# Optimization experiments

Hardware: AMD Instinct MI355X
Metric: run time of the kernel (lower is better)

Reference implementation:

```python
import jax, jax.numpy as jnp
import numpy as np

N = 50000      # nodes
E = 800000     # edges (avg degree 16)
D_IN = 128     # in_feats
D_OUT = 128    # out_feats
EPS = 1e-5     # LayerNorm eps


def setup_inputs() -> dict:
    key = jax.random.key(0)
    ks = jax.random.split(key, 8)
    stdv = 1.0 / np.sqrt(5 * D_IN)
    return {
        "h": jax.random.normal(ks[0], (N, D_IN), dtype=jnp.float32),
        "dist": jax.random.uniform(ks[1], (E,), dtype=jnp.float32),
        "W": jax.random.uniform(ks[2], (D_OUT, 5 * D_IN), minval=-stdv, maxval=stdv, dtype=jnp.float32),
        "b": jax.random.uniform(ks[3], (D_OUT,), minval=-stdv, maxval=stdv, dtype=jnp.float32),
        "gamma": jnp.ones((D_OUT,), dtype=jnp.float32),
        "beta": jnp.zeros((D_OUT,), dtype=jnp.float32),
        "src": jax.random.randint(ks[4], (E,), 0, N, dtype=jnp.int32),
        "dst": jax.random.randint(ks[5], (E,), 0, N, dtype=jnp.int32),
        "positions": jax.random.randint(ks[6], (E,), 0, 4, dtype=jnp.int32),
    }


def reference(h, dist, W, b, gamma, beta, src, dst, positions):
    n = h.shape[0]
    h_src = h[src]  # [E, D] gather once, reused by all four directions

    def direction(p):
        # edge-masked u_mul_e + sum aggregation to dst
        w = jnp.where(positions == p, dist, 0.0)
        return jax.ops.segment_sum(h_src * w[:, None], dst, num_segments=n)

    r = direction(0)   # right
    bt = direction(1)  # bottom
    l = direction(2)   # left
    t = direction(0)   # top (original code reuses positions == 0 — faithful)

    cat = jnp.concatenate([h, r, bt, l, t], axis=1)  # [N, 5D]
    z = cat @ W.T + b                                 # [N, D_OUT]
    mu = jnp.mean(z, axis=-1, keepdims=True)
    var = jnp.mean(jnp.square(z - mu), axis=-1, keepdims=True)
    z = (z - mu) * jax.lax.rsqrt(var + EPS) * gamma + beta
    return jax.nn.relu(z)
```

## Files before the change

### kernel.cpp

```cpp
#include <hip/hip_runtime.h>
#include <math.h>
#include <stdint.h>

constexpr int NN = 50000;
constexpr int EE = 800000;
constexpr int D  = 128;
constexpr int KK = 512;
constexpr int KA = 384;
constexpr int BM = 64;
constexpr int BK = 64;
constexpr int NPAD = 50048;
constexpr int CAP = 64;

typedef __attribute__((ext_vector_type(8)))  short bf16x8;
typedef __attribute__((ext_vector_type(16))) float f32x16;

__device__ inline unsigned short f2bf(float x) {
    unsigned u = __builtin_bit_cast(unsigned, x);
    unsigned r = (u + 0x7FFF + ((u >> 16) & 1)) >> 16;
    return (unsigned short)r;
}
__device__ inline float bf2f(unsigned short b) {
    unsigned u = ((unsigned)b) << 16;
    return __builtin_bit_cast(float, u);
}

__global__ __launch_bounds__(256) void prep_wfrag(const float* __restrict__ W,
                                                  unsigned short* __restrict__ Wfh,
                                                  unsigned short* __restrict__ Wfl)
{
    int tid = blockIdx.x * 256 + threadIdx.x;
    int ln  = tid & 31;
    int ksl = (tid >> 5) & 63;
    int cb  = tid >> 11;
    int col = cb * 32 + ln;
    short h8[8], l8[8];
#pragma unroll
    for (int j = 0; j < 8; ++j) {
        int k = ksl * 8 + j;
        float v = W[col * 640 + k];
        if (k >= 128 && k < 256) v += W[col * 640 + k + 384];
        unsigned short hb = f2bf(v);
        h8[j] = (short)hb;
        l8[j] = (short)f2bf(v - bf2f(hb));
    }
    *(bf16x8*)(Wfh + (size_t)tid * 8) = *(bf16x8*)h8;
    *(bf16x8*)(Wfl + (size_t)tid * 8) = *(bf16x8*)l8;
}

__global__ __launch_bounds__(256) void fill_bucket(const int* __restrict__ src,
                                                   const int* __restrict__ dst,
                                                   const int* __restrict__ pos,
                                                   const float* __restrict__ dist,
                                                   int* __restrict__ deg,
                                                   int2* __restrict__ bucket)
{
    int e = blockIdx.x * 256 + threadIdx.x;
    if (e >= EE) return;
    int p = pos[e];
    if (p == 3) return;
    int d_ = dst[e];
    int slot = atomicAdd(&deg[d_], 1);
    if (slot < CAP)
        bucket[(size_t)d_ * CAP + slot] =
            make_int2(src[e] | (p << 16), __float_as_int(dist[e]));
}

__global__ __launch_bounds__(256) void gather_agg(const float* __restrict__ h,
                                                  const int2* __restrict__ bucket,
                                                  const int* __restrict__ deg,
                                                  unsigned short* __restrict__ Xhi)
{
    int node = (blockIdx.x * 256 + threadIdx.x) >> 6;
    if (node >= NN) return;
    int lane = threadIdx.x & 63;
    int n = deg[node];
    if (n > CAP) n = CAP;

    int2 mreg = (lane < n) ? bucket[(size_t)node * CAP + lane] : make_int2(0, 0);

    float2 a0 = {0.f, 0.f}, a1 = {0.f, 0.f}, a2 = {0.f, 0.f};
    int e = 0;
    for (; e + 8 <= n; e += 8) {
        float2 v[8];
        float  wq[8];
        int    pq[8];
#pragma unroll
        for (int j = 0; j < 8; ++j) {
            int mx = __shfl(mreg.x, e + j);
            int my = __shfl(mreg.y, e + j);
            pq[j] = mx >> 16;
            wq[j] = __int_as_float(my);
            v[j]  = ((const float2*)(h + (size_t)(mx & 0xFFFF) * D))[lane];
        }
#pragma unroll
        for (int j = 0; j < 8; ++j) {
            float w0 = (pq[j] == 0) ? wq[j] : 0.f;
            float w1 = (pq[j] == 1) ? wq[j] : 0.f;
            float w2 = (pq[j] == 2) ? wq[j] : 0.f;
            a0.x = fmaf(v[j].x, w0, a0.x); a0.y = fmaf(v[j].y, w0, a0.y);
            a1.x = fmaf(v[j].x, w1, a1.x); a1.y = fmaf(v[j].y, w1, a1.y);
            a2.x = fmaf(v[j].x, w2, a2.x); a2.y = fmaf(v[j].y, w2, a2.y);
        }
    }
    for (; e < n; ++e) {
        int mx = __shfl(mreg.x, e);
        int my = __shfl(mreg.y, e);
        float w = __int_as_float(my);
        float2 v = ((const float2*)(h + (size_t)(mx & 0xFFFF) * D))[lane];
        float w0 = ((mx >> 16) == 0) ? w : 0.f;
        float w1 = ((mx >> 16) == 1) ? w : 0.f;
        float w2 = ((mx >> 16) == 2) ? w : 0.f;
        a0.x = fmaf(v.x, w0, a0.x); a0.y = fmaf(v.y, w0, a0.y);
        a1.x = fmaf(v.x, w1, a1.x); a1.y = fmaf(v.y, w1, a1.y);
        a2.x = fmaf(v.x, w2, a2.x); a2.y = fmaf(v.y, w2, a2.y);
    }

    size_t base = (size_t)node * KA + lane * 2;
    float2 as[3] = {a0, a1, a2};
#pragma unroll
    for (int p = 0; p < 3; ++p) {
        unsigned short h0 = f2bf(as[p].x), h1 = f2bf(as[p].y);
        *(unsigned*)(Xhi + base + p * 128) = (unsigned)h0 | ((unsigned)h1 << 16);
    }
}

__global__ __launch_bounds__(256, 3) void gemm_mfma(
    const float* __restrict__ h,
    const unsigned short* __restrict__ Xhi,
    const unsigned short* __restrict__ Wfh, const unsigned short* __restrict__ Wfl,
    const float* __restrict__ bias, const float* __restrict__ gamma,
    const float* __restrict__ beta, float* __restrict__ out)
{
    __shared__ __align__(16) short lds[2 * BM * BK];

    const int t = threadIdx.x;
    const int l = t & 63;
    const int w = t >> 6;
    const int wr = (w & 1) * 32;
    const int wch = (w >> 1);
    const int row0 = blockIdx.x * BM;
    const int ln = l & 31;
    const int hs = l >> 5;

    int crow[2], cks[2], clof[2];
#pragma unroll
    for (int p = 0; p < 2; ++p) {
        int idx = t + 256 * p;
        crow[p] = idx >> 3;
        cks[p]  = idx & 7;
        clof[p] = crow[p] * 64 + ((cks[p] ^ (crow[p] & 7)) * 8);
    }

    float4 pa[4];

    auto LOADA = [&](int kt) {
        const int k0 = kt * BK;
        if (kt < 2) {
#pragma unroll
            for (int p = 0; p < 2; ++p) {
                int grow = row0 + crow[p];
                if (grow < NN) {
                    const float* hp = h + (size_t)grow * D + k0 + cks[p] * 8;
                    pa[2 * p]     = *(const float4*)hp;
                    pa[2 * p + 1] = *(const float4*)(hp + 4);
                } else {
                    pa[2 * p]     = make_float4(0, 0, 0, 0);
                    pa[2 * p + 1] = make_float4(0, 0, 0, 0);
                }
            }
        } else {
#pragma unroll
            for (int p = 0; p < 2; ++p) {
                size_t ga = (size_t)(row0 + crow[p]) * KA + (k0 - 128) + cks[p] * 8;
                pa[p] = *(const float4*)(Xhi + ga);
            }
        }
    };

    auto STOREA = [&](int kt, short* buf) {
        if (kt < 2) {
#pragma unroll
            for (int p = 0; p < 2; ++p) {
                const float* f0 = (const float*)&pa[2 * p];
                const float* f1 = (const float*)&pa[2 * p + 1];
                short b8[8];
#pragma unroll
                for (int j = 0; j < 4; ++j) {
                    b8[j]     = (short)f2bf(f0[j]);
                    b8[4 + j] = (short)f2bf(f1[j]);
                }
                *(bf16x8*)(buf + clof[p]) = *(bf16x8*)b8;
            }
        } else {
#pragma unroll
            for (int p = 0; p < 2; ++p)
                *(float4*)(buf + clof[p]) = pa[p];
        }
    };

    f32x16 acc[2];
#pragma unroll
    for (int cb = 0; cb < 2; ++cb)
#pragma unroll
        for (int i = 0; i < 16; ++i) acc[cb][i] = 0.f;

    LOADA(0);
    STOREA(0, lds);
    LOADA(1);
    __syncthreads();

    for (int kt = 0; kt < 8; ++kt) {
        short* buf = lds + (kt & 1) * BM * BK;
        bf16x8 bfh[2][4], bfl[2][4];
#pragma unroll
        for (int cb = 0; cb < 2; ++cb)
#pragma unroll
            for (int kk = 0; kk < 4; ++kk) {
                size_t fo = ((size_t)((wch * 2 + cb) * 64 + kt * 8 + kk * 2 + hs)
                             * 32 + ln) * 8;
                bfh[cb][kk] = *(const bf16x8*)(Wfh + fo);
                bfl[cb][kk] = *(const bf16x8*)(Wfl + fo);
            }
        if (kt < 7) STOREA(kt + 1, lds + ((kt + 1) & 1) * BM * BK);
        if (kt < 6) LOADA(kt + 2);

        __builtin_amdgcn_s_setprio(1);
#pragma unroll
        for (int kk = 0; kk < 4; ++kk) {
            int ksl = kk * 2 + hs;
            int row = wr + ln;
            bf16x8 a = *(const bf16x8*)(buf + row * 64 + ((ksl ^ (row & 7)) * 8));
#pragma unroll
            for (int cb = 0; cb < 2; ++cb) {
                acc[cb] = __builtin_amdgcn_mfma_f32_32x32x16_bf16(
                    a, bfh[cb][kk], acc[cb], 0, 0, 0);
                acc[cb] = __builtin_amdgcn_mfma_f32_32x32x16_bf16(
                    a, bfl[cb][kk], acc[cb], 0, 0, 0);
            }
        }
        __builtin_amdgcn_s_setprio(0);
        __syncthreads();
    }

    float* part = (float*)lds;
    float bias_c[2] = {bias[wch * 64 + ln], bias[wch * 64 + 32 + ln]};

#pragma unroll
    for (int reg = 0; reg < 16; ++reg) {
        float z0 = acc[0][reg] + bias_c[0];
        float z1 = acc[1][reg] + bias_c[1];
        acc[0][reg] = z0;
        acc[1][reg] = z1;
        float s = z0 + z1, ss = z0 * z0 + z1 * z1;
#pragma unroll
        for (int m = 1; m < 32; m <<= 1) {
            s  += __shfl_xor(s, m, 64);
            ss += __shfl_xor(ss, m, 64);
        }
        int rl = wr + (reg & 3) + 8 * (reg >> 2) + 4 * hs;
        if (ln == 0) {
            part[wch * 128 + rl * 2]     = s;
            part[wch * 128 + rl * 2 + 1] = ss;
        }
    }
    __syncthreads();

    float g_c[2]  = {gamma[wch * 64 + ln], gamma[wch * 64 + 32 + ln]};
    float be_c[2] = {beta[wch * 64 + ln],  beta[wch * 64 + 32 + ln]};
#pragma unroll
    for (int reg = 0; reg < 16; ++reg) {
        int rl = wr + (reg & 3) + 8 * (reg >> 2) + 4 * hs;
        float s  = part[rl * 2]     + part[128 + rl * 2];
        float ss = part[rl * 2 + 1] + part[128 + rl * 2 + 1];
        float mu  = s * (1.f / 128.f);
        float var = ss * (1.f / 128.f) - mu * mu;
        float rs  = rsqrtf(var + 1e-5f);
        int grow = row0 + rl;
        if (grow < NN) {
            float v0 = (acc[0][reg] - mu) * rs * g_c[0] + be_c[0];
            float v1 = (acc[1][reg] - mu) * rs * g_c[1] + be_c[1];
            out[(size_t)grow * D + wch * 64 + ln]      = v0 > 0.f ? v0 : 0.f;
            out[(size_t)grow * D + wch * 64 + 32 + ln] = v1 > 0.f ? v1 : 0.f;
        }
    }
}

extern "C" void kernel_launch(void* const* d_in, const int* in_sizes, int n_in,
                              void* d_out, int out_size, void* d_ws, size_t ws_size,
                              hipStream_t stream)
{
    const float* h     = (const float*)d_in[0];
    const float* dist  = (const float*)d_in[1];
    const float* W     = (const float*)d_in[2];
    const float* bias  = (const float*)d_in[3];
    const float* gamma = (const float*)d_in[4];
    const float* beta  = (const float*)d_in[5];
    const int*   src   = (const int*)d_in[6];
    const int*   dst   = (const int*)d_in[7];
    const int*   pos   = (const int*)d_in[8];

    unsigned short* Xhi = (unsigned short*)d_ws;
    unsigned short* Wfh = Xhi + (size_t)NPAD * KA;
    unsigned short* Wfl = Wfh + 128 * KK;
    int*  deg    = (int*)(Wfl + 128 * KK);
    int2* bucket = (int2*)(((uintptr_t)(deg + NN) + 15) & ~(uintptr_t)15);

    hipMemsetAsync(deg, 0, NN * sizeof(int), stream);

    prep_wfrag<<<32, 256, 0, stream>>>(W, Wfh, Wfl);
    fill_bucket<<<(EE + 255) / 256, 256, 0, stream>>>(src, dst, pos, dist, deg, bucket);
    gather_agg<<<(NN * 64) / 256, 256, 0, stream>>>(h, bucket, deg, Xhi);
    gemm_mfma<<<NPAD / BM, 256, 0, stream>>>(h, Xhi, Wfh, Wfl, bias, gamma,
                                             beta, (float*)d_out);
}
```

Measured before the change: 208.4 us.

## Pre-convert h to bf16 in unified activation buffer and widen gather loads

A new kernel converts h to bf16 and writes it into the first 128 columns of a single 512-wide bf16 activation matrix. The GEMM then streams every K tile uniformly from that matrix, with no fp32 load and conversion branch. The gather kernel now has each half-wave process alternate edges with float4 loads, then combines the two halves with a cross-lane xor shuffle and splits the stores between them. This costs an extra launch and an extra bf16 write and read of h, in exchange for a simpler GEMM inner loop and wider gather loads.

```diff
diff --git a/kernel.cpp b/kernel.cpp
--- a/kernel.cpp
+++ b/kernel.cpp
@@ -6,7 +6,6 @@
 constexpr int EE = 800000;
 constexpr int D  = 128;
 constexpr int KK = 512;
-constexpr int KA = 384;
 constexpr int BM = 64;
 constexpr int BK = 64;
 constexpr int NPAD = 50048;
@@ -23,6 +22,22 @@
 __device__ inline float bf2f(unsigned short b) {
     unsigned u = ((unsigned)b) << 16;
     return __builtin_bit_cast(float, u);
+}
+
+__global__ __launch_bounds__(256) void h2bf16(const float* __restrict__ h,
+                                              unsigned short* __restrict__ Xfull)
+{
+    int idx = blockIdx.x * 256 + threadIdx.x;
+    int n  = idx >> 4;
+    int c8 = (idx & 15) * 8;
+    const float* hp = h + (size_t)n * D + c8;
+    float4 f0 = *(const float4*)hp;
+    float4 f1 = *(const float4*)(hp + 4);
+    float ff[8] = {f0.x, f0.y, f0.z, f0.w, f1.x, f1.y, f1.z, f1.w};
+    short b8[8];
+#pragma unroll
+    for (int j = 0; j < 8; ++j) b8[j] = (short)f2bf(ff[j]);
+    *(bf16x8*)(Xfull + (size_t)n * KK + c8) = *(bf16x8*)b8;
 }
 
 __global__ __launch_bounds__(256) void prep_wfrag(const float* __restrict__ W,
@@ -69,65 +84,76 @@
 __global__ __launch_bounds__(256) void gather_agg(const float* __restrict__ h,
                                                   const int2* __restrict__ bucket,
                                                   const int* __restrict__ deg,
-                                                  unsigned short* __restrict__ Xhi)
+                                                  unsigned short* __restrict__ Xfull)
 {
     int node = (blockIdx.x * 256 + threadIdx.x) >> 6;
     if (node >= NN) return;
     int lane = threadIdx.x & 63;
+    int hs = lane >> 5;
+    int c0 = (lane & 31) * 4;
     int n = deg[node];
     if (n > CAP) n = CAP;
 
     int2 mreg = (lane < n) ? bucket[(size_t)node * CAP + lane] : make_int2(0, 0);
 
-    float2 a0 = {0.f, 0.f}, a1 = {0.f, 0.f}, a2 = {0.f, 0.f};
-    int e = 0;
-    for (; e + 8 <= n; e += 8) {
-        float2 v[8];
+    float a0[4] = {0.f, 0.f, 0.f, 0.f};
+    float a1[4] = {0.f, 0.f, 0.f, 0.f};
+    float a2[4] = {0.f, 0.f, 0.f, 0.f};
+
+    for (int base = 0; base < n; base += 16) {
+        float4 v[8];
         float  wq[8];
         int    pq[8];
 #pragma unroll
         for (int j = 0; j < 8; ++j) {
-            int mx = __shfl(mreg.x, e + j);
-            int my = __shfl(mreg.y, e + j);
+            int idx = base + 2 * j + hs;
+            bool pred = idx < n;
+            int mx = __shfl(mreg.x, idx & 63, 64);
+            int my = __shfl(mreg.y, idx & 63, 64);
             pq[j] = mx >> 16;
-            wq[j] = __int_as_float(my);
-            v[j]  = ((const float2*)(h + (size_t)(mx & 0xFFFF) * D))[lane];
+            wq[j] = pred ? __int_as_float(my) : 0.f;
+            const float* hp = h + (size_t)(mx & 0xFFFF) * D + c0;
+            v[j] = pred ? *(const float4*)hp : make_float4(0.f, 0.f, 0.f, 0.f);
         }
 #pragma unroll
         for (int j = 0; j < 8; ++j) {
             float w0 = (pq[j] == 0) ? wq[j] : 0.f;
             float w1 = (pq[j] == 1) ? wq[j] : 0.f;
             float w2 = (pq[j] == 2) ? wq[j] : 0.f;
-            a0.x = fmaf(v[j].x, w0, a0.x); a0.y = fmaf(v[j].y, w0, a0.y);
-            a1.x = fmaf(v[j].x, w1, a1.x); a1.y = fmaf(v[j].y, w1, a1.y);
-            a2.x = fmaf(v[j].x, w2, a2.x); a2.y = fmaf(v[j].y, w2, a2.y);
-        }
-    }
-    for (; e < n; ++e) {
-        int mx = __shfl(mreg.x, e);
-        int my = __shfl(mreg.y, e);
-        float w = __int_as_float(my);
-        float2 v = ((const float2*)(h + (size_t)(mx & 0xFFFF) * D))[lane];
-        float w0 = ((mx >> 16) == 0) ? w : 0.f;
-        float w1 = ((mx >> 16) == 1) ? w : 0.f;
-        float w2 = ((mx >> 16) == 2) ? w : 0.f;
-        a0.x = fmaf(v.x, w0, a0.x); a0.y = fmaf(v.y, w0, a0.y);
-        a1.x = fmaf(v.x, w1, a1.x); a1.y = fmaf(v.y, w1, a1.y);
-        a2.x = fmaf(v.x, w2, a2.x); a2.y = fmaf(v.y, w2, a2.y);
-    }
-
-    size_t base = (size_t)node * KA + lane * 2;
-    float2 as[3] = {a0, a1, a2};
-#pragma unroll
-    for (int p = 0; p < 3; ++p) {
-        unsigned short h0 = f2bf(as[p].x), h1 = f2bf(as[p].y);
-        *(unsigned*)(Xhi + base + p * 128) = (unsigned)h0 | ((unsigned)h1 << 16);
+            float vv[4] = {v[j].x, v[j].y, v[j].z, v[j].w};
+#pragma unroll
+            for (int c = 0; c < 4; ++c) {
+                a0[c] = fmaf(vv[c], w0, a0[c]);
+                a1[c] = fmaf(vv[c], w1, a1[c]);
+                a2[c] = fmaf(vv[c], w2, a2[c]);
+            }
+        }
+    }
+
+#pragma unroll
+    for (int c = 0; c < 4; ++c) {
+        a0[c] += __shfl_xor(a0[c], 32, 64);
+        a1[c] += __shfl_xor(a1[c], 32, 64);
+        a2[c] += __shfl_xor(a2[c], 32, 64);
+    }
+
+    size_t rowb = (size_t)node * KK;
+    if (hs == 0) {
+        uint2 w0 = make_uint2((unsigned)f2bf(a0[0]) | ((unsigned)f2bf(a0[1]) << 16),
+                              (unsigned)f2bf(a0[2]) | ((unsigned)f2bf(a0[3]) << 16));
+        uint2 w1 = make_uint2((unsigned)f2bf(a1[0]) | ((unsigned)f2bf(a1[1]) << 16),
+                              (unsigned)f2bf(a1[2]) | ((unsigned)f2bf(a1[3]) << 16));
+        *(uint2*)(Xfull + rowb + 128 + c0) = w0;
+        *(uint2*)(Xfull + rowb + 256 + c0) = w1;
+    } else {
+        uint2 w2 = make_uint2((unsigned)f2bf(a2[0]) | ((unsigned)f2bf(a2[1]) << 16),
+                              (unsigned)f2bf(a2[2]) | ((unsigned)f2bf(a2[3]) << 16));
+        *(uint2*)(Xfull + rowb + 384 + c0) = w2;
     }
 }
 
 __global__ __launch_bounds__(256, 3) void gemm_mfma(
-    const float* __restrict__ h,
-    const unsigned short* __restrict__ Xhi,
+    const unsigned short* __restrict__ Xfull,
     const unsigned short* __restrict__ Wfh, const unsigned short* __restrict__ Wfl,
     const float* __restrict__ bias, const float* __restrict__ gamma,
     const float* __restrict__ beta, float* __restrict__ out)
@@ -152,51 +178,20 @@
         clof[p] = crow[p] * 64 + ((cks[p] ^ (crow[p] & 7)) * 8);
     }
 
-    float4 pa[4];
+    float4 pa[2];
 
     auto LOADA = [&](int kt) {
         const int k0 = kt * BK;
-        if (kt < 2) {
-#pragma unroll
-            for (int p = 0; p < 2; ++p) {
-                int grow = row0 + crow[p];
-                if (grow < NN) {
-                    const float* hp = h + (size_t)grow * D + k0 + cks[p] * 8;
-                    pa[2 * p]     = *(const float4*)hp;
-                    pa[2 * p + 1] = *(const float4*)(hp + 4);
-                } else {
-                    pa[2 * p]     = make_float4(0, 0, 0, 0);
-                    pa[2 * p + 1] = make_float4(0, 0, 0, 0);
-                }
-            }
-        } else {
-#pragma unroll
-            for (int p = 0; p < 2; ++p) {
-                size_t ga = (size_t)(row0 + crow[p]) * KA + (k0 - 128) + cks[p] * 8;
-                pa[p] = *(const float4*)(Xhi + ga);
-            }
+#pragma unroll
+        for (int p = 0; p < 2; ++p) {
+            size_t ga = (size_t)(row0 + crow[p]) * KK + k0 + cks[p] * 8;
+            pa[p] = *(const float4*)(Xfull + ga);
         }
     };
-
-    auto STOREA = [&](int kt, short* buf) {
-        if (kt < 2) {
-#pragma unroll
-            for (int p = 0; p < 2; ++p) {
-                const float* f0 = (const float*)&pa[2 * p];
-                const float* f1 = (const float*)&pa[2 * p + 1];
-                short b8[8];
-#pragma unroll
-                for (int j = 0; j < 4; ++j) {
-                    b8[j]     = (short)f2bf(f0[j]);
-                    b8[4 + j] = (short)f2bf(f1[j]);
-                }
-                *(bf16x8*)(buf + clof[p]) = *(bf16x8*)b8;
-            }
-        } else {
-#pragma unroll
-            for (int p = 0; p < 2; ++p)
-                *(float4*)(buf + clof[p]) = pa[p];
-        }
+    auto STOREA = [&](short* buf) {
+#pragma unroll
+        for (int p = 0; p < 2; ++p)
+            *(float4*)(buf + clof[p]) = pa[p];
     };
 
     f32x16 acc[2];
@@ -206,7 +201,7 @@
         for (int i = 0; i < 16; ++i) acc[cb][i] = 0.f;
 
     LOADA(0);
-    STOREA(0, lds);
+    STOREA(lds);
     LOADA(1);
     __syncthreads();
 
@@ -222,7 +217,7 @@
                 bfh[cb][kk] = *(const bf16x8*)(Wfh + fo);
                 bfl[cb][kk] = *(const bf16x8*)(Wfl + fo);
             }
-        if (kt < 7) STOREA(kt + 1, lds + ((kt + 1) & 1) * BM * BK);
+        if (kt < 7) STOREA(lds + ((kt + 1) & 1) * BM * BK);
         if (kt < 6) LOADA(kt + 2);
 
         __builtin_amdgcn_s_setprio(1);
@@ -300,17 +295,18 @@
     const int*   dst   = (const int*)d_in[7];
     const int*   pos   = (const int*)d_in[8];
 
-    unsigned short* Xhi = (unsigned short*)d_ws;
-    unsigned short* Wfh = Xhi + (size_t)NPAD * KA;
+    unsigned short* Xfull = (unsigned short*)d_ws;
+    unsigned short* Wfh = Xfull + (size_t)NPAD * KK;
     unsigned short* Wfl = Wfh + 128 * KK;
     int*  deg    = (int*)(Wfl + 128 * KK);
     int2* bucket = (int2*)(((uintptr_t)(deg + NN) + 15) & ~(uintptr_t)15);
 
     hipMemsetAsync(deg, 0, NN * sizeof(int), stream);
 
+    h2bf16<<<(NN * 16) / 256, 256, 0, stream>>>(h, Xfull);
     prep_wfrag<<<32, 256, 0, stream>>>(W, Wfh, Wfl);
     fill_bucket<<<(EE + 255) / 256, 256, 0, stream>>>(src, dst, pos, dist, deg, bucket);
-    gather_agg<<<(NN * 64) / 256, 256, 0, stream>>>(h, bucket, deg, Xhi);
-    gemm_mfma<<<NPAD / BM, 256, 0, stream>>>(h, Xhi, Wfh, Wfl, bias, gamma,
+    gather_agg<<<(NN * 64) / 256, 256, 0, stream>>>(h, bucket, deg, Xfull);
+    gemm_mfma<<<NPAD / BM, 256, 0, stream>>>(Xfull, Wfh, Wfl, bias, gamma,
                                              beta, (float*)d_out);
 }
```

Measured after the change: 227.8 us. 9.3% more time.
